# Kernel optimization log

Measured on AMD Instinct MI355X. Metric: run time of the kernel, lower is better.

Reference implementation:

```python
import jax, jax.numpy as jnp
import numpy as np

B, T, D, H = 4, 2048, 1024, 16
HD = D // H
SCALE = D ** (-0.5)  # note: module scales by d_model**-0.5, not head_dim**-0.5


def setup_inputs() -> dict:
    key = jax.random.key(0)
    k1, k2, k3 = jax.random.split(key, 3)
    x = jax.random.normal(k1, (B, T, D), dtype=jnp.float32)
    Wqkv = jax.random.normal(k2, (D, 3 * D), dtype=jnp.float32) * (D ** -0.5)
    Wo = jax.random.normal(k3, (D, D), dtype=jnp.float32) * (D ** -0.5)
    return {"x": x, "Wqkv": Wqkv, "Wo": Wo}


def reference(x, Wqkv, Wo):
    b, t, c = x.shape
    qkv = x @ Wqkv  # [B,T,3D]
    q, k, v = jnp.split(qkv, 3, axis=-1)
    q = q.reshape(b, t, H, HD).transpose(0, 2, 1, 3)  # [B,H,T,HD]
    k = k.reshape(b, t, H, HD).transpose(0, 2, 1, 3)
    v = v.reshape(b, t, H, HD).transpose(0, 2, 1, 3)
    attn = jnp.einsum('bhid,bhjd->bhij', q, k) * SCALE  # [B,H,T,T]
    mask = jnp.tril(jnp.ones((t, t), dtype=jnp.bool_))
    attn = jnp.where(mask[None, None], attn, jnp.finfo(attn.dtype).min)
    attn = jax.nn.softmax(attn, axis=-1)
    out = jnp.einsum('bhij,bhjd->bhid', attn, v)  # [B,H,T,HD]
    out = out.transpose(0, 2, 1, 3).reshape(b, t, c)
    return out @ Wo
```

## Files before the change

kernel.cpp:

```cpp
#include <hip/hip_runtime.h>
#include <hip/hip_bf16.h>

#define B_ 4
#define T_ 2048
#define D_ 1024
#define H_ 16
#define HD_ 64

typedef __bf16 bf16;
typedef __bf16 bf16x8 __attribute__((ext_vector_type(8)));
typedef __bf16 bf16x4 __attribute__((ext_vector_type(4)));
typedef float f32x4 __attribute__((ext_vector_type(4)));
typedef float f32x16 __attribute__((ext_vector_type(16)));

#define MFMA16(a, b, c) __builtin_amdgcn_mfma_f32_16x16x32_bf16(a, b, c, 0, 0, 0)
#define MFMA32(a, b, c) __builtin_amdgcn_mfma_f32_32x32x16_bf16(a, b, c, 0, 0, 0)

__device__ inline void gld_lds16(const bf16* g, bf16* l) {
  __builtin_amdgcn_global_load_lds((const __attribute__((address_space(1))) void*)g,
                                   (__attribute__((address_space(3))) void*)l, 16, 0, 0);
}

__device__ inline unsigned pkbf16(float a, float b) {
  unsigned r;
  asm("v_cvt_pk_bf16_f32 %0, %1, %2" : "=v"(r) : "v"(a), "v"(b));
  return r;
}
__device__ inline void pl32swap(unsigned& x, unsigned& y) {
  asm("v_permlane32_swap_b32 %0, %1" : "+v"(x), "+v"(y));
}

#define PACKJ(dst, S, base)                        \
  {                                                \
    unsigned w0 = pkbf16(S[base + 0], S[base + 1]); \
    unsigned w2 = pkbf16(S[base + 4], S[base + 5]); \
    pl32swap(w0, w2);                              \
    unsigned w1 = pkbf16(S[base + 2], S[base + 3]); \
    unsigned w3 = pkbf16(S[base + 6], S[base + 7]); \
    pl32swap(w1, w3);                              \
    int4 wi = {(int)w0, (int)w1, (int)w2, (int)w3}; \
    dst = __builtin_bit_cast(bf16x8, wi);          \
  }

__global__ void cvt_f32_bf16(const float* __restrict__ in, bf16* __restrict__ out) {
  int i = (blockIdx.x * 256 + threadIdx.x) * 8;
  float4 v0 = *(const float4*)(in + i);
  float4 v1 = *(const float4*)(in + i + 4);
  bf16x8 o = {(bf16)v0.x, (bf16)v0.y, (bf16)v0.z, (bf16)v0.w,
              (bf16)v1.x, (bf16)v1.y, (bf16)v1.z, (bf16)v1.w};
  *(bf16x8*)(out + i) = o;
}

__global__ void transpose_f32_bf16(const float* __restrict__ in, bf16* __restrict__ out,
                                   int R, int C) {
  __shared__ float tile[32][33];
  int c0 = blockIdx.x * 32, r0 = blockIdx.y * 32;
  int tx = threadIdx.x, ty = threadIdx.y;
#pragma unroll
  for (int i = 0; i < 4; i++)
    tile[ty + i * 8][tx] = in[(size_t)(r0 + ty + i * 8) * C + c0 + tx];
  __syncthreads();
#pragma unroll
  for (int i = 0; i < 4; i++)
    out[(size_t)(c0 + ty + i * 8) * R + r0 + tx] = (bf16)tile[tx][ty + i * 8];
}

__global__ __launch_bounds__(256) void transpose_v(const bf16* __restrict__ in,
                                                   bf16* __restrict__ out) {
  __shared__ bf16 tile[64 * 72];
  int bh = blockIdx.y;
  int t0 = blockIdx.x * 64;
  int tid = threadIdx.x;
  const bf16* ib = in + (size_t)bh * T_ * HD_;
  bf16* ob = out + (size_t)bh * HD_ * T_;
  int lr = tid >> 3, lc = (tid & 7) * 8;
#pragma unroll
  for (int it = 0; it < 2; it++) {
    bf16x8 v = *(const bf16x8*)(ib + (size_t)(t0 + lr + it * 32) * HD_ + lc);
#pragma unroll
    for (int e = 0; e < 8; e++) tile[(lr + it * 32) * 72 + lc + e] = v[e];
  }
  __syncthreads();
#pragma unroll
  for (int it = 0; it < 2; it++) {
    int d = (tid >> 3) + it * 32;
    bf16x8 v;
#pragma unroll
    for (int e = 0; e < 8; e++) v[e] = tile[((tid & 7) * 8 + e) * 72 + d];
    *(bf16x8*)(ob + (size_t)d * T_ + t0 + (tid & 7) * 8) = v;
  }
}

template <int EPI>
__global__ __launch_bounds__(256) void gemm_bt(const bf16* __restrict__ A,
                                               const bf16* __restrict__ Bt,
                                               bf16* __restrict__ qb, bf16* __restrict__ kb,
                                               bf16* __restrict__ vb, float* __restrict__ fout,
                                               int M, int N, int K) {
  __shared__ __align__(16) bf16 lds_a[2][128 * 32];
  __shared__ __align__(16) bf16 lds_b[2][128 * 32];
  int n0 = blockIdx.x * 128, m0 = blockIdx.y * 128;
  int tid = threadIdx.x, wave = tid >> 6, lane = tid & 63;
  int l16 = lane & 15, lhi = lane >> 4;
  int wr = wave >> 1, wc = wave & 1;
  f32x4 acc[4][4];
#pragma unroll
  for (int mt = 0; mt < 4; mt++)
#pragma unroll
    for (int nt = 0; nt < 4; nt++) acc[mt][nt] = (f32x4){0.f, 0.f, 0.f, 0.f};

  int sr = wave * 16 + (lane >> 2);
  int scol = (lane & 3) * 8;
  const bf16* ga = A + (size_t)(m0 + sr) * K + scol;
  const bf16* gb = Bt + (size_t)(n0 + sr) * K + scol;

  auto STAGE = [&](int buf, int k0) {
    gld_lds16(ga + k0, &lds_a[buf][wave * 512]);
    gld_lds16(ga + (size_t)64 * K + k0, &lds_a[buf][2048 + wave * 512]);
    gld_lds16(gb + k0, &lds_b[buf][wave * 512]);
    gld_lds16(gb + (size_t)64 * K + k0, &lds_b[buf][2048 + wave * 512]);
  };

  int NT = K >> 5;
  STAGE(0, 0);
  STAGE(1, 32);
  for (int t = 0; t < NT; t++) {
    if (t + 1 < NT)
      asm volatile("s_waitcnt vmcnt(4)" ::: "memory");
    else
      asm volatile("s_waitcnt vmcnt(0)" ::: "memory");
    __builtin_amdgcn_s_barrier();
    const bf16* la = lds_a[t & 1];
    const bf16* lb = lds_b[t & 1];
    bf16x8 af[4], bfr[4];
#pragma unroll
    for (int mt = 0; mt < 4; mt++)
      af[mt] = *(const bf16x8*)&la[(wr * 64 + mt * 16 + l16) * 32 + 8 * lhi];
#pragma unroll
    for (int nt = 0; nt < 4; nt++)
      bfr[nt] = *(const bf16x8*)&lb[(wc * 64 + nt * 16 + l16) * 32 + 8 * lhi];
    asm volatile("s_waitcnt lgkmcnt(0)" ::: "memory");
    __builtin_amdgcn_s_barrier();
    if (t + 2 < NT) STAGE(t & 1, (t + 2) * 32);
    __builtin_amdgcn_s_setprio(1);
#pragma unroll
    for (int mt = 0; mt < 4; mt++)
#pragma unroll
      for (int nt = 0; nt < 4; nt++) acc[mt][nt] = MFMA16(af[mt], bfr[nt], acc[mt][nt]);
    __builtin_amdgcn_s_setprio(0);
  }

  if (EPI == 0) {
    __syncthreads();
    int col0 = n0 + wc * 64;
    int sec = col0 >> 10;
    int h = (col0 & 1023) >> 6;
    bf16* dst = (sec == 0) ? qb : (sec == 1 ? kb : vb);
    float scale = (sec == 0) ? 0.045084439f : 1.f;
    bf16* scr = ((bf16*)lds_a) + wave * 1168;
#pragma unroll
    for (int mt = 0; mt < 4; mt++) {
#pragma unroll
      for (int nt = 0; nt < 4; nt++)
#pragma unroll
        for (int rr = 0; rr < 4; rr++)
          scr[(4 * lhi + rr) * 72 + nt * 16 + l16] = (bf16)(acc[mt][nt][rr] * scale);
#pragma unroll
      for (int p = 0; p < 2; p++) {
        int r16 = p * 8 + (lane >> 3);
        int c8 = (lane & 7) * 8;
        bf16x8 v = *(const bf16x8*)(scr + r16 * 72 + c8);
        int row = m0 + wr * 64 + mt * 16 + r16;
        int b = row >> 11, tt = row & (T_ - 1);
        *(bf16x8*)(dst + ((size_t)(b * H_ + h) * T_ + tt) * HD_ + c8) = v;
      }
    }
  } else {
#pragma unroll
    for (int mt = 0; mt < 4; mt++)
#pragma unroll
      for (int nt = 0; nt < 4; nt++)
#pragma unroll
        for (int rr = 0; rr < 4; rr++) {
          int row = m0 + wr * 64 + mt * 16 + 4 * lhi + rr;
          int col = n0 + wc * 64 + nt * 16 + l16;
          fout[(size_t)row * N + col] = acc[mt][nt][rr];
        }
  }
}

__global__ __launch_bounds__(256, 4) void attn_kernel(const bf16* __restrict__ qbuf,
                                                      const bf16* __restrict__ kbuf,
                                                      const bf16* __restrict__ vtbuf,
                                                      bf16* __restrict__ obuf) {
  __shared__ __align__(16) bf16 sm[16384];
  int bid = blockIdx.x;
  int bh = (bid & 7) * 8 + ((bid >> 3) & 7);
  const int qtab[16] = {15, 14, 13, 12, 8, 9, 10, 11, 6, 4, 5, 7, 1, 3, 2, 0};
  int qi = qtab[bid >> 6];
  int q0 = qi * 128;
  int wv = threadIdx.x >> 6;
  int lane = threadIdx.x & 63;
  int q = lane & 31, hi = lane >> 5;
  int qw = q0 + wv * 32;
  int b = bh >> 4, h = bh & 15;

  const bf16* Q = qbuf + (size_t)bh * T_ * HD_;
  const bf16* Kg = kbuf + (size_t)bh * T_ * HD_;
  const bf16* Vt = vtbuf + (size_t)bh * HD_ * T_;

  bf16x8 qf[4];
#pragma unroll
  for (int j = 0; j < 4; j++)
    qf[j] = *(const bf16x8*)(Q + (size_t)(qw + q) * HD_ + j * 16 + hi * 8);

  int srow = lane >> 3;
  int sc8 = ((lane & 7) ^ srow) * 8;
  int r0 = wv * 16;
  const bf16* kgp = Kg + (size_t)(r0 + srow) * HD_ + sc8;
  const bf16* vgp = Vt + (size_t)(r0 + srow) * T_ + sc8;

  auto stage = [&](int buf, int t) {
    const bf16* kg = kgp + (size_t)t * 64 * HD_;
    const bf16* vg = vgp + t * 64;
    bf16* kd = sm + buf * 4096;
    bf16* vd = sm + 8192 + buf * 4096;
    gld_lds16(kg, kd + r0 * 64);
    gld_lds16(kg + 8 * HD_, kd + (r0 + 8) * 64);
    gld_lds16(vg, vd + r0 * 64);
    gld_lds16(vg + 8 * T_, vd + (r0 + 8) * 64);
  };

  int xo = (q & 7) << 4;
  int A0 = q * 128 + ((16 * hi) ^ xo);
  int A1 = q * 128 + ((32 + 16 * hi) ^ xo);
  int A2 = q * 128 + ((64 + 16 * hi) ^ xo);
  int A3 = q * 128 + ((96 + 16 * hi) ^ xo);
  const char* smc = (const char*)sm;

  f32x16 o1, o2;
#pragma unroll
  for (int r = 0; r < 16; r++) {
    o1[r] = 0.f;
    o2[r] = 0.f;
  }
  f32x16 zro;
#pragma unroll
  for (int r = 0; r < 16; r++) zro[r] = 0.f;
  float l_r = 0.f;
  const float MFIX = 12.f;
  int ntm = 2 * qi + 2;

  stage(0, 0);
  stage(1, 1);
  for (int t = 0; t < ntm; ++t) {
    if (t + 1 < ntm)
      asm volatile("s_waitcnt vmcnt(4)" ::: "memory");
    else
      asm volatile("s_waitcnt vmcnt(0)" ::: "memory");
    __builtin_amdgcn_s_barrier();
    int KB = (t & 1) * 8192;
    int VB = 16384 + (t & 1) * 8192;
    int jb = t * 64;
    bool active = (jb <= qw + 31);
    bf16x8 pf0, pf1, pf2, pf3;
    bf16x8 vf0, vf1, vf2, vf3, vf4, vf5, vf6, vf7;
    if (active) {
      bf16x8 kf[8];
      kf[0] = *(const bf16x8*)(smc + KB + A0);
      kf[1] = *(const bf16x8*)(smc + KB + A1);
      kf[2] = *(const bf16x8*)(smc + KB + A2);
      kf[3] = *(const bf16x8*)(smc + KB + A3);
      kf[4] = *(const bf16x8*)(smc + KB + 4096 + A0);
      kf[5] = *(const bf16x8*)(smc + KB + 4096 + A1);
      kf[6] = *(const bf16x8*)(smc + KB + 4096 + A2);
      kf[7] = *(const bf16x8*)(smc + KB + 4096 + A3);
      f32x16 s1, s2;
      __builtin_amdgcn_s_setprio(1);
      s1 = MFMA32(kf[0], qf[0], zro);
#pragma unroll
      for (int j = 1; j < 4; j++) s1 = MFMA32(kf[j], qf[j], s1);
      s2 = MFMA32(kf[4], qf[0], zro);
#pragma unroll
      for (int j = 1; j < 4; j++) s2 = MFMA32(kf[4 + j], qf[j], s2);
      __builtin_amdgcn_s_setprio(0);
      if (jb + 63 > qw) {
#pragma unroll
        for (int r = 0; r < 16; r++) {
          int kv = (r & 3) + 8 * (r >> 2) + 4 * hi;
          if (jb + kv > qw + q) s1[r] = -1e30f;
          if (jb + kv + 32 > qw + q) s2[r] = -1e30f;
        }
      }
#pragma unroll
      for (int r = 0; r < 16; r++) s1[r] = exp2f(s1[r] - MFIX);
#pragma unroll
      for (int r = 0; r < 16; r++) s2[r] = exp2f(s2[r] - MFIX);
      float ts[8];
#pragma unroll
      for (int r = 0; r < 8; r++) ts[r] = (s1[r] + s1[r + 8]) + (s2[r] + s2[r + 8]);
#pragma unroll
      for (int r = 0; r < 4; r++) ts[r] += ts[r + 4];
      float su = (ts[0] + ts[1]) + (ts[2] + ts[3]);
      su += __shfl_xor(su, 32);
      l_r += su;
      PACKJ(pf0, s1, 0);
      PACKJ(pf1, s1, 8);
      PACKJ(pf2, s2, 0);
      PACKJ(pf3, s2, 8);
      vf0 = *(const bf16x8*)(smc + VB + A0);
      vf1 = *(const bf16x8*)(smc + VB + A1);
      vf2 = *(const bf16x8*)(smc + VB + A2);
      vf3 = *(const bf16x8*)(smc + VB + A3);
      vf4 = *(const bf16x8*)(smc + VB + 4096 + A0);
      vf5 = *(const bf16x8*)(smc + VB + 4096 + A1);
      vf6 = *(const bf16x8*)(smc + VB + 4096 + A2);
      vf7 = *(const bf16x8*)(smc + VB + 4096 + A3);
    }
    asm volatile("s_waitcnt lgkmcnt(0)" ::: "memory");
    __builtin_amdgcn_s_barrier();
    if (t + 2 < ntm) stage(t & 1, t + 2);
    if (active) {
      __builtin_amdgcn_s_setprio(1);
      o1 = MFMA32(vf0, pf0, o1);
      o2 = MFMA32(vf4, pf0, o2);
      o1 = MFMA32(vf1, pf1, o1);
      o2 = MFMA32(vf5, pf1, o2);
      o1 = MFMA32(vf2, pf2, o1);
      o2 = MFMA32(vf6, pf2, o2);
      o1 = MFMA32(vf3, pf3, o1);
      o2 = MFMA32(vf7, pf3, o2);
      __builtin_amdgcn_s_setprio(0);
    }
  }
  __syncthreads();

  bf16* scr = sm + wv * 2112;
  float inv = 1.f / l_r;
#pragma unroll
  for (int r = 0; r < 16; r++) {
    int d = (r & 3) + 8 * (r >> 2) + 4 * hi;
    scr[d * 33 + q] = (bf16)(o1[r] * inv);
    scr[(32 + d) * 33 + q] = (bf16)(o2[r] * inv);
  }
#pragma unroll
  for (int pass = 0; pass < 4; pass++) {
    int row = qw + pass * 8 + (lane >> 3);
    int dcol = (lane & 7) * 8;
    bf16x8 ov;
#pragma unroll
    for (int e = 0; e < 8; e++) ov[e] = scr[(dcol + e) * 33 + pass * 8 + (lane >> 3)];
    *(bf16x8*)(obuf + ((size_t)(b * T_ + row)) * D_ + h * 64 + dcol) = ov;
  }
}

extern "C" void kernel_launch(void* const* d_in, const int* in_sizes, int n_in, void* d_out,
                              int out_size, void* d_ws, size_t ws_size, hipStream_t stream) {
  const float* x = (const float*)d_in[0];
  const float* wqkv = (const float*)d_in[1];
  const float* wo = (const float*)d_in[2];
  float* out = (float*)d_out;
  char* ws = (char*)d_ws;

  bf16* xb = (bf16*)ws;
  bf16* wqkvt = (bf16*)(ws + (16u << 20));
  bf16* wot = (bf16*)(ws + (22u << 20));
  bf16* qb = (bf16*)(ws + (24u << 20));
  bf16* kb = (bf16*)(ws + (40u << 20));
  bf16* vb = (bf16*)(ws + (56u << 20));
  bf16* vtb = (bf16*)(ws + (72u << 20));
  bf16* ao = (bf16*)(ws + (88u << 20));

  cvt_f32_bf16<<<4096, 256, 0, stream>>>(x, xb);
  transpose_f32_bf16<<<dim3(96, 32), dim3(32, 8), 0, stream>>>(wqkv, wqkvt, 1024, 3072);
  transpose_f32_bf16<<<dim3(32, 32), dim3(32, 8), 0, stream>>>(wo, wot, 1024, 1024);
  gemm_bt<0><<<dim3(24, 64), 256, 0, stream>>>(xb, wqkvt, qb, kb, vb, nullptr,
                                               B_ * T_, 3 * D_, D_);
  transpose_v<<<dim3(32, 64), 256, 0, stream>>>(vb, vtb);
  attn_kernel<<<1024, 256, 0, stream>>>(qb, kb, vtb, ao);
  gemm_bt<1><<<dim3(8, 64), 256, 0, stream>>>(ao, wot, nullptr, nullptr, nullptr, out,
                                              B_ * T_, D_, D_);
}
```

Measured before the change: 179.0 us.

## Fuse V transpose into QKV GEMM epilogue and remap block order

The separate transpose_v kernel is removed. The QKV GEMM epilogue now writes V directly in [B,H,HD,T] layout by reading the LDS scratch tile column-wise, which saves one kernel launch and a full read/write pass over V. Blocks now use a 1D grid with a remapped index so that consecutive blocks walk M first (a swizzle of the 64 M-tiles) while sharing the same N tile, aiming for better L2 reuse of weights. The transposed V store writes 16 contiguous bf16 per lane across strided rows, so its global write coalescing is worse than before.

```diff
diff --git a/kernel.cpp b/kernel.cpp
--- a/kernel.cpp
+++ b/kernel.cpp
@@ -65,41 +65,17 @@
     out[(size_t)(c0 + ty + i * 8) * R + r0 + tx] = (bf16)tile[tx][ty + i * 8];
 }
 
-__global__ __launch_bounds__(256) void transpose_v(const bf16* __restrict__ in,
-                                                   bf16* __restrict__ out) {
-  __shared__ bf16 tile[64 * 72];
-  int bh = blockIdx.y;
-  int t0 = blockIdx.x * 64;
-  int tid = threadIdx.x;
-  const bf16* ib = in + (size_t)bh * T_ * HD_;
-  bf16* ob = out + (size_t)bh * HD_ * T_;
-  int lr = tid >> 3, lc = (tid & 7) * 8;
-#pragma unroll
-  for (int it = 0; it < 2; it++) {
-    bf16x8 v = *(const bf16x8*)(ib + (size_t)(t0 + lr + it * 32) * HD_ + lc);
-#pragma unroll
-    for (int e = 0; e < 8; e++) tile[(lr + it * 32) * 72 + lc + e] = v[e];
-  }
-  __syncthreads();
-#pragma unroll
-  for (int it = 0; it < 2; it++) {
-    int d = (tid >> 3) + it * 32;
-    bf16x8 v;
-#pragma unroll
-    for (int e = 0; e < 8; e++) v[e] = tile[((tid & 7) * 8 + e) * 72 + d];
-    *(bf16x8*)(ob + (size_t)d * T_ + t0 + (tid & 7) * 8) = v;
-  }
-}
-
 template <int EPI>
 __global__ __launch_bounds__(256) void gemm_bt(const bf16* __restrict__ A,
                                                const bf16* __restrict__ Bt,
                                                bf16* __restrict__ qb, bf16* __restrict__ kb,
-                                               bf16* __restrict__ vb, float* __restrict__ fout,
+                                               bf16* __restrict__ vtb, float* __restrict__ fout,
                                                int M, int N, int K) {
   __shared__ __align__(16) bf16 lds_a[2][128 * 32];
   __shared__ __align__(16) bf16 lds_b[2][128 * 32];
-  int n0 = blockIdx.x * 128, m0 = blockIdx.y * 128;
+  int bid = blockIdx.x;
+  int m0 = ((bid & 7) * 8 + ((bid >> 3) & 7)) * 128;
+  int n0 = (bid >> 6) * 128;
   int tid = threadIdx.x, wave = tid >> 6, lane = tid & 63;
   int l16 = lane & 15, lhi = lane >> 4;
   int wr = wave >> 1, wc = wave & 1;
@@ -155,7 +131,6 @@
     int col0 = n0 + wc * 64;
     int sec = col0 >> 10;
     int h = (col0 & 1023) >> 6;
-    bf16* dst = (sec == 0) ? qb : (sec == 1 ? kb : vb);
     float scale = (sec == 0) ? 0.045084439f : 1.f;
     bf16* scr = ((bf16*)lds_a) + wave * 1168;
 #pragma unroll
@@ -165,14 +140,28 @@
 #pragma unroll
         for (int rr = 0; rr < 4; rr++)
           scr[(4 * lhi + rr) * 72 + nt * 16 + l16] = (bf16)(acc[mt][nt][rr] * scale);
-#pragma unroll
-      for (int p = 0; p < 2; p++) {
-        int r16 = p * 8 + (lane >> 3);
-        int c8 = (lane & 7) * 8;
-        bf16x8 v = *(const bf16x8*)(scr + r16 * 72 + c8);
-        int row = m0 + wr * 64 + mt * 16 + r16;
-        int b = row >> 11, tt = row & (T_ - 1);
-        *(bf16x8*)(dst + ((size_t)(b * H_ + h) * T_ + tt) * HD_ + c8) = v;
+      int row0 = m0 + wr * 64 + mt * 16;
+      int b = row0 >> 11, tt0 = row0 & (T_ - 1);
+      if (sec != 2) {
+        bf16* dst = (sec == 0) ? qb : kb;
+#pragma unroll
+        for (int p = 0; p < 2; p++) {
+          int r16 = p * 8 + (lane >> 3);
+          int c8 = (lane & 7) * 8;
+          bf16x8 v = *(const bf16x8*)(scr + r16 * 72 + c8);
+          *(bf16x8*)(dst + ((size_t)(b * H_ + h) * T_ + tt0 + r16) * HD_ + c8) = v;
+        }
+      } else {
+        int d = lane;
+        bf16x8 v0, v1;
+#pragma unroll
+        for (int e = 0; e < 8; e++) {
+          v0[e] = scr[e * 72 + d];
+          v1[e] = scr[(8 + e) * 72 + d];
+        }
+        bf16* vt = vtb + ((size_t)(b * H_ + h) * HD_ + d) * T_ + tt0;
+        *(bf16x8*)(vt) = v0;
+        *(bf16x8*)(vt + 8) = v1;
       }
     }
   } else {
@@ -367,17 +356,13 @@
   bf16* wot = (bf16*)(ws + (22u << 20));
   bf16* qb = (bf16*)(ws + (24u << 20));
   bf16* kb = (bf16*)(ws + (40u << 20));
-  bf16* vb = (bf16*)(ws + (56u << 20));
   bf16* vtb = (bf16*)(ws + (72u << 20));
   bf16* ao = (bf16*)(ws + (88u << 20));
 
   cvt_f32_bf16<<<4096, 256, 0, stream>>>(x, xb);
   transpose_f32_bf16<<<dim3(96, 32), dim3(32, 8), 0, stream>>>(wqkv, wqkvt, 1024, 3072);
   transpose_f32_bf16<<<dim3(32, 32), dim3(32, 8), 0, stream>>>(wo, wot, 1024, 1024);
-  gemm_bt<0><<<dim3(24, 64), 256, 0, stream>>>(xb, wqkvt, qb, kb, vb, nullptr,
-                                               B_ * T_, 3 * D_, D_);
-  transpose_v<<<dim3(32, 64), 256, 0, stream>>>(vb, vtb);
+  gemm_bt<0><<<1536, 256, 0, stream>>>(xb, wqkvt, qb, kb, vtb, nullptr, B_ * T_, 3 * D_, D_);
   attn_kernel<<<1024, 256, 0, stream>>>(qb, kb, vtb, ao);
-  gemm_bt<1><<<dim3(8, 64), 256, 0, stream>>>(ao, wot, nullptr, nullptr, nullptr, out,
-                                              B_ * T_, D_, D_);
-}
+  gemm_bt<1><<<512, 256, 0, stream>>>(ao, wot, nullptr, nullptr, nullptr, out, B_ * T_, D_, D_);
+}
```

Result: faster. 169.7 us (-5.2%).
